# Performance work log

Measured on AMD Instinct MI355X. Metric: run time of the kernel, lower is better.

## Reference

```python
import jax, jax.numpy as jnp
import numpy as np

HIDDEN_DIM = 1024
NUM_HEADS = 16
HEAD_DIM = HIDDEN_DIM // NUM_HEADS
SCALAR_NORM = float(np.sqrt(HIDDEN_DIM / NUM_HEADS))


def setup_inputs() -> dict:
    key = jax.random.key(0)
    k1, k2 = jax.random.split(key)
    B, N, D = 2, 2048, HIDDEN_DIM
    x = jax.random.normal(k1, (B, N, D), dtype=jnp.float32)
    # torch Linear weight shape: (3D, D); xavier_uniform-like scale
    limit = float(np.sqrt(6.0 / (D + 3 * D)))
    W_qkv = jax.random.uniform(k2, (3 * D, D), dtype=jnp.float32, minval=-limit, maxval=limit)
    return {"x": x, "W_qkv": W_qkv}


def reference(x, W_qkv):
    b, n, d = x.shape
    h, hd = NUM_HEADS, HEAD_DIM
    qkv = x @ W_qkv.T  # (B, N, 3D)
    q, k, v = jnp.split(qkv, 3, axis=-1)
    # (B, H, N, hd)
    q = q.reshape(b, n, h, hd).transpose(0, 2, 1, 3)
    k = k.reshape(b, n, h, hd).transpose(0, 2, 1, 3)
    v = v.reshape(b, n, h, hd).transpose(0, 2, 1, 3)
    scores = jnp.einsum('bhik,bhjk->bhij', q, k) / SCALAR_NORM
    attn = jax.nn.softmax(scores, axis=-1)
    out = jnp.einsum('bhij,bhjk->bhik', attn, v)
    return out.transpose(0, 2, 1, 3).reshape(b, n, d)
```

## Files before the change

kernel.cpp:

```cpp
#include <hip/hip_runtime.h>
#include <hip/hip_bf16.h>

#define SEQ 2048
#define DMODEL 1024
#define NHEADS 16
#define HD 64
#define BATCH 2

typedef short bf16x8 __attribute__((ext_vector_type(8)));
typedef float f32x4 __attribute__((ext_vector_type(4)));
typedef float f32x16 __attribute__((ext_vector_type(16)));

static __device__ inline ushort f2bf(float f) {
    unsigned u = __float_as_uint(f);
    return (ushort)((u + 0x7fffu + ((u >> 16) & 1u)) >> 16);
}

static __device__ inline unsigned pk2bf(float a, float b) {
    __hip_bfloat162 h = __float22bfloat162_rn(make_float2(a, b));
    union { __hip_bfloat162 h; unsigned u; } c; c.h = h;
    return c.u;
}

static __device__ inline void async16(const ushort* g, ushort* l) {
    __builtin_amdgcn_global_load_lds((const __attribute__((address_space(1))) void*)g,
                                     (__attribute__((address_space(3))) void*)l, 16, 0, 0);
}

static __device__ inline void plane32swap(unsigned& a, unsigned& b) {
    asm volatile("v_permlane32_swap_b32 %0, %1" : "+v"(a), "+v"(b));
}

__global__ void cvt2(const float* __restrict__ a, ushort* __restrict__ da, int na,
                     const float* __restrict__ b, ushort* __restrict__ db, int nb) {
    long i = (long)(blockIdx.x * blockDim.x + threadIdx.x) * 4;
    const float* s; ushort* d;
    if (i < na) { s = a + i; d = da + i; }
    else { long j = i - na; if (j >= nb) return; s = b + j; d = db + j; }
    float4 v = *(const float4*)s;
    ushort4 o; o.x = f2bf(v.x); o.y = f2bf(v.y); o.z = f2bf(v.z); o.w = f2bf(v.w);
    *(ushort4*)d = o;
}

union GemmSmem {
    struct { ushort A[128 * 64]; ushort B[128 * 64]; } st;
    ushort C[128 * 128];
};

__global__ __launch_bounds__(256) void qkv_gemm(
        const ushort* __restrict__ X, const ushort* __restrict__ W,
        ushort* __restrict__ Qd, ushort* __restrict__ Kd, ushort* __restrict__ Vd) {
    __shared__ GemmSmem sm;
    const int t = threadIdx.x;
    const int lane = t & 63, l15 = lane & 15, quad = lane >> 4;
    const int w = t >> 6, wm = w >> 1, wn = w & 1;
    const int gm = blockIdx.x, gn = blockIdx.y;
    const int srow = t >> 3, scol = (t & 7) * 8;

    f32x4 acc[4][4] = {};

    for (int kt = 0; kt < 16; ++kt) {
        const int k0 = kt * 64;
        __syncthreads();
#pragma unroll
        for (int inst = 0; inst < 4; ++inst) {
            async16(&X[(gm * 128 + inst * 32 + srow) * 1024 + k0 + scol], &sm.st.A[inst * 2048 + t * 8]);
            async16(&W[(gn * 128 + inst * 32 + srow) * 1024 + k0 + scol], &sm.st.B[inst * 2048 + t * 8]);
        }
        __syncthreads();
#pragma unroll
        for (int ks = 0; ks < 2; ++ks) {
            const int kk = ks * 32 + quad * 8;
            bf16x8 af[4], bfr[4];
#pragma unroll
            for (int i = 0; i < 4; ++i) {
                af[i]  = *(const bf16x8*)&sm.st.A[(wm * 64 + i * 16 + l15) * 64 + kk];
                bfr[i] = *(const bf16x8*)&sm.st.B[(wn * 64 + i * 16 + l15) * 64 + kk];
            }
#pragma unroll
            for (int i = 0; i < 4; ++i)
#pragma unroll
                for (int j = 0; j < 4; ++j)
                    acc[i][j] = __builtin_amdgcn_mfma_f32_16x16x32_bf16(af[i], bfr[j], acc[i][j], 0, 0, 0);
        }
    }

    __syncthreads();
    const float sc = (gn < 8) ? (0.125f * 1.44269504f) : 1.0f;
#pragma unroll
    for (int i = 0; i < 4; ++i)
#pragma unroll
        for (int reg = 0; reg < 4; ++reg) {
            const int row = wm * 64 + i * 16 + quad * 4 + reg;
            const int sw = (row & 7) * 8;
#pragma unroll
            for (int jp = 0; jp < 4; jp += 2) {
                unsigned u = pk2bf(acc[i][jp][reg] * sc, acc[i][jp + 1][reg] * sc);
                sm.C[row * 128 + ((wn * 64 + jp * 16 + l15) ^ sw)] = (ushort)u;
                sm.C[row * 128 + ((wn * 64 + (jp + 1) * 16 + l15) ^ sw)] = (ushort)(u >> 16);
            }
        }
    __syncthreads();

    const int which = gn >> 3;
    ushort* dst = (which == 0) ? Qd : ((which == 1) ? Kd : Vd);
    const int rloc = t >> 4, l = t & 15;
#pragma unroll
    for (int pass = 0; pass < 8; ++pass) {
        const int r = pass * 16 + rloc;
        bf16x8 v = *(const bf16x8*)&sm.C[r * 128 + ((l * 8) ^ ((r & 7) * 8))];
        const int ng = gm * 128 + r;
        const int b = ng >> 11, n = ng & 2047;
        const int cl = (gn * 128 + l * 8) & 1023;
        const int h = cl >> 6, hd = cl & 63;
        *(bf16x8*)&dst[(((b * NHEADS + h) * SEQ) + n) * HD + hd] = v;
    }
}

__global__ __launch_bounds__(256) void tr_v(const ushort* __restrict__ src, ushort* __restrict__ dst) {
    __shared__ ushort sT[64][72];
    const int t = threadIdx.x;
    const int bh = blockIdx.y, nt = blockIdx.x;
    const int r0 = t >> 3, c8 = (t & 7) * 8;
    const ushort* sp = src + ((long)bh * SEQ + nt * 64) * HD;
#pragma unroll
    for (int rr = 0; rr < 64; rr += 32)
        *(bf16x8*)&sT[rr + r0][c8] = *(const bf16x8*)&sp[(rr + r0) * HD + c8];
    __syncthreads();
    ushort* dp = dst + (long)bh * HD * SEQ + nt * 64;
#pragma unroll
    for (int rr = 0; rr < 64; rr += 32) {
        const int hd = rr + r0;
        bf16x8 v;
#pragma unroll
        for (int j = 0; j < 8; ++j) v[j] = (short)sT[c8 + j][hd];
        *(bf16x8*)&dp[(long)hd * SEQ + c8] = v;
    }
}

__global__ __launch_bounds__(256, 1) void attn_kernel(
        const ushort* __restrict__ Q, const ushort* __restrict__ K,
        const ushort* __restrict__ VT, float* __restrict__ O) {
    __shared__ ushort sK[2][128 * 64];
    __shared__ ushort sVT[2][64 * 128];
    __shared__ float sL[4][64];

    const int t = threadIdx.x;
    const int lane = t & 63, l31 = lane & 31, hi = lane >> 5;
    const int w = t >> 6;

    const int flat = blockIdx.y * gridDim.x + blockIdx.x;
    const int qt = (flat >> 3) & 7;
    const int bh = (flat & 7) + ((flat >> 6) << 3);

    const ushort* Qp = Q + ((long)bh * SEQ + qt * 256 + w * 64) * HD;
    const ushort* Kp = K + (long)bh * SEQ * HD;
    const ushort* Vp = VT + (long)bh * HD * SEQ;

    bf16x8 bq[2][4];
#pragma unroll
    for (int qh = 0; qh < 2; ++qh)
#pragma unroll
        for (int ks = 0; ks < 4; ++ks)
            bq[qh][ks] = *(const bf16x8*)&Qp[(qh * 32 + l31) * HD + ks * 16 + hi * 8];

    const int krow = t >> 3;
    const int kcol = ((t & 7) ^ (krow & 7)) * 8;
    const ushort* gK = Kp + krow * HD + kcol;
    const int vrow = t >> 4;
    const int vcol = ((t & 15) ^ (vrow & 7)) * 8;
    const ushort* gV = Vp + (long)vrow * SEQ + vcol;

    ushort* lK[2] = { &sK[0][t * 8], &sK[1][t * 8] };
    ushort* lV[2] = { &sVT[0][t * 8], &sVT[1][t * 8] };

    f32x16 accA[2] = {}, accB[2] = {};
    f32x4 LpA = {}, LpB = {};
    const int swz = (l31 & 7) << 3;

#pragma unroll
    for (int c = 0; c < 4; ++c) {
        async16(gK + c * 32 * HD, lK[0] + c * 2048);
        async16(gV + (long)c * 16 * SEQ, lV[0] + c * 2048);
    }
    __syncthreads();

    for (int kt = 0; kt < 16; ++kt) {
        const int cur = kt & 1;
        if (kt < 15) {
            const ushort* nK = gK + (kt + 1) * 128 * HD;
            const ushort* nV = gV + (kt + 1) * 128;
#pragma unroll
            for (int c = 0; c < 4; ++c) {
                async16(nK + c * 32 * HD, lK[cur ^ 1] + c * 2048);
                async16(nV + (long)c * 16 * SEQ, lV[cur ^ 1] + c * 2048);
            }
        }
        const ushort* bK = sK[cur];
        const ushort* bV = sVT[cur];

        f32x16 sA[4], sB[4];
#pragma unroll
        for (int nb = 0; nb < 4; ++nb) {
            f32x16 zA = {}, zB = {};
#pragma unroll
            for (int ks = 0; ks < 4; ++ks) {
                bf16x8 ak = *(const bf16x8*)&bK[(nb * 32 + l31) * 64 + ((ks * 16 + hi * 8) ^ swz)];
                zA = __builtin_amdgcn_mfma_f32_32x32x16_bf16(ak, bq[0][ks], zA, 0, 0, 0);
                zB = __builtin_amdgcn_mfma_f32_32x32x16_bf16(ak, bq[1][ks], zB, 0, 0, 0);
            }
            sA[nb] = zA; sB[nb] = zB;
        }

#pragma unroll
        for (int h = 0; h < 2; ++h) {
            bf16x8 paA[4], paB[4];
#pragma unroll
            for (int nb2 = 0; nb2 < 2; ++nb2) {
                float pA[16], pB[16];
#pragma unroll
                for (int r = 0; r < 16; ++r) {
                    pA[r] = __builtin_amdgcn_exp2f(sA[h * 2 + nb2][r]);
                    pB[r] = __builtin_amdgcn_exp2f(sB[h * 2 + nb2][r]);
                }
#pragma unroll
                for (int r = 0; r < 16; ++r) { LpA[r & 3] += pA[r]; LpB[r & 3] += pB[r]; }
#pragma unroll
                for (int h2 = 0; h2 < 2; ++h2) {
                    const int b = 8 * h2;
                    unsigned a0 = pk2bf(pA[b + 0], pA[b + 1]);
                    unsigned a1 = pk2bf(pA[b + 2], pA[b + 3]);
                    unsigned a2 = pk2bf(pA[b + 4], pA[b + 5]);
                    unsigned a3 = pk2bf(pA[b + 6], pA[b + 7]);
                    plane32swap(a0, a2);
                    plane32swap(a1, a3);
                    union { unsigned u[4]; bf16x8 v; } fa;
                    fa.u[0] = a0; fa.u[1] = a1; fa.u[2] = a2; fa.u[3] = a3;
                    paA[nb2 * 2 + h2] = fa.v;
                    unsigned b0 = pk2bf(pB[b + 0], pB[b + 1]);
                    unsigned b1 = pk2bf(pB[b + 2], pB[b + 3]);
                    unsigned b2 = pk2bf(pB[b + 4], pB[b + 5]);
                    unsigned b3 = pk2bf(pB[b + 6], pB[b + 7]);
                    plane32swap(b0, b2);
                    plane32swap(b1, b3);
                    union { unsigned u[4]; bf16x8 v; } fb;
                    fb.u[0] = b0; fb.u[1] = b1; fb.u[2] = b2; fb.u[3] = b3;
                    paB[nb2 * 2 + h2] = fb.v;
                }
            }
#pragma unroll
            for (int db = 0; db < 2; ++db)
#pragma unroll
                for (int ks = 0; ks < 4; ++ks) {
                    bf16x8 vf = *(const bf16x8*)&bV[(db * 32 + l31) * 128 + h * 64 + ((ks * 16 + hi * 8) ^ swz)];
                    accA[db] = __builtin_amdgcn_mfma_f32_32x32x16_bf16(paA[ks], vf, accA[db], 0, 0, 0);
                    accB[db] = __builtin_amdgcn_mfma_f32_32x32x16_bf16(paB[ks], vf, accB[db], 0, 0, 0);
                }
        }

        __syncthreads();
    }

    {
        const float la = (LpA[0] + LpA[1]) + (LpA[2] + LpA[3]);
        unsigned lu = __float_as_uint(la), lv = lu;
        plane32swap(lu, lv);
        const float lb = (LpB[0] + LpB[1]) + (LpB[2] + LpB[3]);
        unsigned mu = __float_as_uint(lb), mv = mu;
        plane32swap(mu, mv);
        if (hi == 0) {
            sL[w][l31]      = __uint_as_float(lu) + __uint_as_float(lv);
            sL[w][32 + l31] = __uint_as_float(mu) + __uint_as_float(mv);
        }
    }
    __syncthreads();

    const int b = bh >> 4, h = bh & 15;
    const int qg0 = qt * 256 + w * 64;
#pragma unroll
    for (int r = 0; r < 16; ++r) {
        const int ql = (r & 3) + 8 * (r >> 2) + 4 * hi;
        const float invA = 1.0f / sL[w][ql];
        const float invB = 1.0f / sL[w][32 + ql];
#pragma unroll
        for (int db = 0; db < 2; ++db) {
            O[((long)b * SEQ + qg0 + ql) * DMODEL + h * HD + db * 32 + l31]      = accA[db][r] * invA;
            O[((long)b * SEQ + qg0 + 32 + ql) * DMODEL + h * HD + db * 32 + l31] = accB[db][r] * invB;
        }
    }
}

extern "C" void kernel_launch(void* const* d_in, const int* in_sizes, int n_in,
                              void* d_out, int out_size, void* d_ws, size_t ws_size,
                              hipStream_t stream) {
    const float* x  = (const float*)d_in[0];
    const float* Wq = (const float*)d_in[1];
    float* out = (float*)d_out;

    const int NX = BATCH * SEQ * DMODEL;
    const int NW = 3 * DMODEL * DMODEL;
    const int NQKV = BATCH * NHEADS * SEQ * HD;

    ushort* xb = (ushort*)d_ws;
    ushort* wb = xb + NX;
    ushort* q  = wb + NW;
    ushort* k  = q + NQKV;
    ushort* vtmp = k + NQKV;
    ushort* vt = xb;

    cvt2<<<(NX + NW) / 4 / 256, 256, 0, stream>>>(x, xb, NX, Wq, wb, NW);

    dim3 g1(4096 / 128, 3072 / 128);
    qkv_gemm<<<g1, 256, 0, stream>>>(xb, wb, q, k, vtmp);

    dim3 gt(SEQ / 64, BATCH * NHEADS);
    tr_v<<<gt, 256, 0, stream>>>(vtmp, vt);

    dim3 g2(SEQ / 256, BATCH * NHEADS);
    attn_kernel<<<g2, 256, 0, stream>>>(q, k, vt, out);
}
```

Before: 170.1 us.

## Triple-buffer K/V tiles and software-pipeline QK with softmax/PV

Moves K and V shared-memory staging from double to triple buffering, prefetching two tiles ahead with explicit vmcnt waits and raw s_barrier instead of __syncthreads. The loop is restructured so the QK^T MFMAs for the next tile are issued after the softmax and PV of the current tile, which lets the tensor work of one tile overlap the exp work of another. This is meant to hide global-load latency and the serialization between exp and MFMA phases within a single wave. In exchange it uses more LDS (48KB of K/V), holds all eight P fragments live, and raises register pressure. The final iterations redundantly refetch tile 15 to keep the vmcnt accounting uniform.

```diff
diff --git a/kernel.cpp b/kernel.cpp
--- a/kernel.cpp
+++ b/kernel.cpp
@@ -141,8 +141,8 @@
 __global__ __launch_bounds__(256, 1) void attn_kernel(
         const ushort* __restrict__ Q, const ushort* __restrict__ K,
         const ushort* __restrict__ VT, float* __restrict__ O) {
-    __shared__ ushort sK[2][128 * 64];
-    __shared__ ushort sVT[2][64 * 128];
+    __shared__ ushort sK[3][128 * 64];
+    __shared__ ushort sVT[3][64 * 128];
     __shared__ float sL[4][64];
 
     const int t = threadIdx.x;
@@ -171,35 +171,28 @@
     const int vcol = ((t & 15) ^ (vrow & 7)) * 8;
     const ushort* gV = Vp + (long)vrow * SEQ + vcol;
 
-    ushort* lK[2] = { &sK[0][t * 8], &sK[1][t * 8] };
-    ushort* lV[2] = { &sVT[0][t * 8], &sVT[1][t * 8] };
+    ushort* stK0 = &sK[0][t * 8]; ushort* stK1 = &sK[1][t * 8]; ushort* stK2 = &sK[2][t * 8];
+    ushort* stV0 = &sVT[0][t * 8]; ushort* stV1 = &sVT[1][t * 8]; ushort* stV2 = &sVT[2][t * 8];
+    const ushort* rdK0 = sK[0]; const ushort* rdK1 = sK[1]; const ushort* rdK2 = sK[2];
+    const ushort* rdV0 = sVT[0]; const ushort* rdV1 = sVT[1]; const ushort* rdV2 = sVT[2];
 
     f32x16 accA[2] = {}, accB[2] = {};
+    f32x16 sA[4], sB[4];
+    bf16x8 paA[8], paB[8];
     f32x4 LpA = {}, LpB = {};
     const int swz = (l31 & 7) << 3;
 
-#pragma unroll
-    for (int c = 0; c < 4; ++c) {
-        async16(gK + c * 32 * HD, lK[0] + c * 2048);
-        async16(gV + (long)c * 16 * SEQ, lV[0] + c * 2048);
-    }
-    __syncthreads();
-
-    for (int kt = 0; kt < 16; ++kt) {
-        const int cur = kt & 1;
-        if (kt < 15) {
-            const ushort* nK = gK + (kt + 1) * 128 * HD;
-            const ushort* nV = gV + (kt + 1) * 128;
-#pragma unroll
-            for (int c = 0; c < 4; ++c) {
-                async16(nK + c * 32 * HD, lK[cur ^ 1] + c * 2048);
-                async16(nV + (long)c * 16 * SEQ, lV[cur ^ 1] + c * 2048);
-            }
-        }
-        const ushort* bK = sK[cur];
-        const ushort* bV = sVT[cur];
-
-        f32x16 sA[4], sB[4];
+    auto do_stage = [&](int tile, ushort* dK, ushort* dV) {
+        const ushort* nK = gK + (long)tile * 128 * HD;
+        const ushort* nV = gV + tile * 128;
+#pragma unroll
+        for (int c = 0; c < 4; ++c) {
+            async16(nK + c * 32 * HD, dK + c * 2048);
+            async16(nV + (long)c * 16 * SEQ, dV + c * 2048);
+        }
+    };
+
+    auto do_qk = [&](const ushort* bK) {
 #pragma unroll
         for (int nb = 0; nb < 4; ++nb) {
             f32x16 zA = {}, zB = {};
@@ -211,55 +204,81 @@
             }
             sA[nb] = zA; sB[nb] = zB;
         }
-
-#pragma unroll
-        for (int h = 0; h < 2; ++h) {
-            bf16x8 paA[4], paB[4];
-#pragma unroll
-            for (int nb2 = 0; nb2 < 2; ++nb2) {
-                float pA[16], pB[16];
-#pragma unroll
-                for (int r = 0; r < 16; ++r) {
-                    pA[r] = __builtin_amdgcn_exp2f(sA[h * 2 + nb2][r]);
-                    pB[r] = __builtin_amdgcn_exp2f(sB[h * 2 + nb2][r]);
-                }
-#pragma unroll
-                for (int r = 0; r < 16; ++r) { LpA[r & 3] += pA[r]; LpB[r & 3] += pB[r]; }
-#pragma unroll
-                for (int h2 = 0; h2 < 2; ++h2) {
-                    const int b = 8 * h2;
-                    unsigned a0 = pk2bf(pA[b + 0], pA[b + 1]);
-                    unsigned a1 = pk2bf(pA[b + 2], pA[b + 3]);
-                    unsigned a2 = pk2bf(pA[b + 4], pA[b + 5]);
-                    unsigned a3 = pk2bf(pA[b + 6], pA[b + 7]);
-                    plane32swap(a0, a2);
-                    plane32swap(a1, a3);
-                    union { unsigned u[4]; bf16x8 v; } fa;
-                    fa.u[0] = a0; fa.u[1] = a1; fa.u[2] = a2; fa.u[3] = a3;
-                    paA[nb2 * 2 + h2] = fa.v;
-                    unsigned b0 = pk2bf(pB[b + 0], pB[b + 1]);
-                    unsigned b1 = pk2bf(pB[b + 2], pB[b + 3]);
-                    unsigned b2 = pk2bf(pB[b + 4], pB[b + 5]);
-                    unsigned b3 = pk2bf(pB[b + 6], pB[b + 7]);
-                    plane32swap(b0, b2);
-                    plane32swap(b1, b3);
-                    union { unsigned u[4]; bf16x8 v; } fb;
-                    fb.u[0] = b0; fb.u[1] = b1; fb.u[2] = b2; fb.u[3] = b3;
-                    paB[nb2 * 2 + h2] = fb.v;
-                }
-            }
+    };
+
+    auto do_sm = [&]() {
+#pragma unroll
+        for (int sb = 0; sb < 4; ++sb) {
+            float pA[16], pB[16];
+#pragma unroll
+            for (int r = 0; r < 16; ++r) {
+                pA[r] = __builtin_amdgcn_exp2f(sA[sb][r]);
+                pB[r] = __builtin_amdgcn_exp2f(sB[sb][r]);
+            }
+#pragma unroll
+            for (int r = 0; r < 16; ++r) { LpA[r & 3] += pA[r]; LpB[r & 3] += pB[r]; }
+#pragma unroll
+            for (int h2 = 0; h2 < 2; ++h2) {
+                const int b = 8 * h2;
+                const int flat = (sb >> 1) * 4 + (sb & 1) * 2 + h2;
+                unsigned a0 = pk2bf(pA[b + 0], pA[b + 1]);
+                unsigned a1 = pk2bf(pA[b + 2], pA[b + 3]);
+                unsigned a2 = pk2bf(pA[b + 4], pA[b + 5]);
+                unsigned a3 = pk2bf(pA[b + 6], pA[b + 7]);
+                plane32swap(a0, a2);
+                plane32swap(a1, a3);
+                union { unsigned u[4]; bf16x8 v; } fa;
+                fa.u[0] = a0; fa.u[1] = a1; fa.u[2] = a2; fa.u[3] = a3;
+                paA[flat] = fa.v;
+                unsigned b0 = pk2bf(pB[b + 0], pB[b + 1]);
+                unsigned b1 = pk2bf(pB[b + 2], pB[b + 3]);
+                unsigned b2 = pk2bf(pB[b + 4], pB[b + 5]);
+                unsigned b3 = pk2bf(pB[b + 6], pB[b + 7]);
+                plane32swap(b0, b2);
+                plane32swap(b1, b3);
+                union { unsigned u[4]; bf16x8 v; } fb;
+                fb.u[0] = b0; fb.u[1] = b1; fb.u[2] = b2; fb.u[3] = b3;
+                paB[flat] = fb.v;
+            }
+        }
+    };
+
+    auto do_pv = [&](const ushort* bV) {
+#pragma unroll
+        for (int h = 0; h < 2; ++h)
 #pragma unroll
             for (int db = 0; db < 2; ++db)
 #pragma unroll
                 for (int ks = 0; ks < 4; ++ks) {
                     bf16x8 vf = *(const bf16x8*)&bV[(db * 32 + l31) * 128 + h * 64 + ((ks * 16 + hi * 8) ^ swz)];
-                    accA[db] = __builtin_amdgcn_mfma_f32_32x32x16_bf16(paA[ks], vf, accA[db], 0, 0, 0);
-                    accB[db] = __builtin_amdgcn_mfma_f32_32x32x16_bf16(paB[ks], vf, accB[db], 0, 0, 0);
+                    accA[db] = __builtin_amdgcn_mfma_f32_32x32x16_bf16(paA[h * 4 + ks], vf, accA[db], 0, 0, 0);
+                    accB[db] = __builtin_amdgcn_mfma_f32_32x32x16_bf16(paB[h * 4 + ks], vf, accB[db], 0, 0, 0);
                 }
-        }
-
-        __syncthreads();
-    }
+    };
+
+    do_stage(0, stK0, stV0);
+    do_stage(1, stK1, stV1);
+    asm volatile("s_waitcnt vmcnt(8)" ::: "memory");
+    __builtin_amdgcn_s_barrier();
+    __builtin_amdgcn_sched_barrier(0);
+    do_qk(rdK0);
+
+    for (int kt = 0; kt < 15; ++kt) {
+        int ft = kt + 2; if (ft > 15) ft = 15;
+        do_stage(ft, stK2, stV2);
+        do_sm();
+        do_pv(rdV0);
+        asm volatile("s_waitcnt vmcnt(8)" ::: "memory");
+        __builtin_amdgcn_s_barrier();
+        __builtin_amdgcn_sched_barrier(0);
+        do_qk(rdK1);
+        ushort* tk = stK0; stK0 = stK1; stK1 = stK2; stK2 = tk;
+        ushort* tv = stV0; stV0 = stV1; stV1 = stV2; stV2 = tv;
+        const ushort* rk = rdK0; rdK0 = rdK1; rdK1 = rdK2; rdK2 = rk;
+        const ushort* rv = rdV0; rdV0 = rdV1; rdV1 = rdV2; rdV2 = rv;
+    }
+    do_sm();
+    do_pv(rdV0);
 
     {
         const float la = (LpA[0] + LpA[1]) + (LpA[2] + LpA[3]);
```

Result: faster. 165.8 us (-2.5%).

## Split attention KV range across two blocks and fuse V transpose into GEMM

Applied to the files above, without the earlier changes.

The QKV GEMM epilogue now writes V directly in transposed (head_dim x seq) layout, which removes the separate transpose kernel. Attention is split in two along the key dimension (split-K / flash-decoding style), doubling the grid to 512 blocks and allowing 2 blocks per CU. Each half writes unnormalized partial outputs and row sums, and a new combine kernel adds the halves and normalizes. This adds an extra fp32 output buffer and a full read/write pass over the output. The split is exact only because the softmax path uses no max subtraction, so the partial sums combine directly.

```diff
diff --git a/kernel.cpp b/kernel.cpp
--- a/kernel.cpp
+++ b/kernel.cpp
@@ -86,64 +86,69 @@
     }
 
     __syncthreads();
-    const float sc = (gn < 8) ? (0.125f * 1.44269504f) : 1.0f;
-#pragma unroll
-    for (int i = 0; i < 4; ++i)
-#pragma unroll
-        for (int reg = 0; reg < 4; ++reg) {
-            const int row = wm * 64 + i * 16 + quad * 4 + reg;
-            const int sw = (row & 7) * 8;
-#pragma unroll
-            for (int jp = 0; jp < 4; jp += 2) {
-                unsigned u = pk2bf(acc[i][jp][reg] * sc, acc[i][jp + 1][reg] * sc);
-                sm.C[row * 128 + ((wn * 64 + jp * 16 + l15) ^ sw)] = (ushort)u;
-                sm.C[row * 128 + ((wn * 64 + (jp + 1) * 16 + l15) ^ sw)] = (ushort)(u >> 16);
-            }
-        }
-    __syncthreads();
-
-    const int which = gn >> 3;
-    ushort* dst = (which == 0) ? Qd : ((which == 1) ? Kd : Vd);
-    const int rloc = t >> 4, l = t & 15;
-#pragma unroll
-    for (int pass = 0; pass < 8; ++pass) {
-        const int r = pass * 16 + rloc;
-        bf16x8 v = *(const bf16x8*)&sm.C[r * 128 + ((l * 8) ^ ((r & 7) * 8))];
-        const int ng = gm * 128 + r;
-        const int b = ng >> 11, n = ng & 2047;
-        const int cl = (gn * 128 + l * 8) & 1023;
-        const int h = cl >> 6, hd = cl & 63;
-        *(bf16x8*)&dst[(((b * NHEADS + h) * SEQ) + n) * HD + hd] = v;
-    }
-}
-
-__global__ __launch_bounds__(256) void tr_v(const ushort* __restrict__ src, ushort* __restrict__ dst) {
-    __shared__ ushort sT[64][72];
-    const int t = threadIdx.x;
-    const int bh = blockIdx.y, nt = blockIdx.x;
-    const int r0 = t >> 3, c8 = (t & 7) * 8;
-    const ushort* sp = src + ((long)bh * SEQ + nt * 64) * HD;
-#pragma unroll
-    for (int rr = 0; rr < 64; rr += 32)
-        *(bf16x8*)&sT[rr + r0][c8] = *(const bf16x8*)&sp[(rr + r0) * HD + c8];
-    __syncthreads();
-    ushort* dp = dst + (long)bh * HD * SEQ + nt * 64;
-#pragma unroll
-    for (int rr = 0; rr < 64; rr += 32) {
-        const int hd = rr + r0;
-        bf16x8 v;
-#pragma unroll
-        for (int j = 0; j < 8; ++j) v[j] = (short)sT[c8 + j][hd];
-        *(bf16x8*)&dp[(long)hd * SEQ + c8] = v;
-    }
-}
-
-__global__ __launch_bounds__(256, 1) void attn_kernel(
+    if (gn < 16) {
+        const float sc = (gn < 8) ? (0.125f * 1.44269504f) : 1.0f;
+#pragma unroll
+        for (int i = 0; i < 4; ++i)
+#pragma unroll
+            for (int reg = 0; reg < 4; ++reg) {
+                const int row = wm * 64 + i * 16 + quad * 4 + reg;
+                const int sw = (row & 7) * 8;
+#pragma unroll
+                for (int jp = 0; jp < 4; jp += 2) {
+                    unsigned u = pk2bf(acc[i][jp][reg] * sc, acc[i][jp + 1][reg] * sc);
+                    sm.C[row * 128 + ((wn * 64 + jp * 16 + l15) ^ sw)] = (ushort)u;
+                    sm.C[row * 128 + ((wn * 64 + (jp + 1) * 16 + l15) ^ sw)] = (ushort)(u >> 16);
+                }
+            }
+        __syncthreads();
+
+        ushort* dst = (gn < 8) ? Qd : Kd;
+        const int rloc = t >> 4, l = t & 15;
+#pragma unroll
+        for (int pass = 0; pass < 8; ++pass) {
+            const int r = pass * 16 + rloc;
+            bf16x8 v = *(const bf16x8*)&sm.C[r * 128 + ((l * 8) ^ ((r & 7) * 8))];
+            const int ng = gm * 128 + r;
+            const int b = ng >> 11, n = ng & 2047;
+            const int cl = (gn * 128 + l * 8) & 1023;
+            const int h = cl >> 6, hd = cl & 63;
+            *(bf16x8*)&dst[(((b * NHEADS + h) * SEQ) + n) * HD + hd] = v;
+        }
+    } else {
+#pragma unroll
+        for (int i = 0; i < 4; ++i)
+#pragma unroll
+            for (int reg = 0; reg < 4; ++reg) {
+                const int nloc = wm * 64 + i * 16 + quad * 4 + reg;
+#pragma unroll
+                for (int jp = 0; jp < 4; ++jp) {
+                    const int f = wn * 64 + jp * 16 + l15;
+                    sm.C[f * 128 + (nloc ^ ((f & 7) * 8))] = f2bf(acc[i][jp][reg]);
+                }
+            }
+        __syncthreads();
+
+        const int rloc = t >> 4, l = t & 15;
+        const int b = gm >> 4;
+        const int n0 = (gm & 15) * 128 + l * 8;
+#pragma unroll
+        for (int pass = 0; pass < 8; ++pass) {
+            const int r = pass * 16 + rloc;
+            bf16x8 v = *(const bf16x8*)&sm.C[r * 128 + ((l * 8) ^ ((r & 7) * 8))];
+            const int cl = (gn * 128 + r) & 1023;
+            const int h = cl >> 6, hd = cl & 63;
+            *(bf16x8*)&Vd[(((long)(b * NHEADS + h) * HD) + hd) * SEQ + n0] = v;
+        }
+    }
+}
+
+__global__ __launch_bounds__(256, 2) void attn_kernel(
         const ushort* __restrict__ Q, const ushort* __restrict__ K,
-        const ushort* __restrict__ VT, float* __restrict__ O) {
+        const ushort* __restrict__ VT, float* __restrict__ O0,
+        float* __restrict__ O1, float* __restrict__ Lbuf) {
     __shared__ ushort sK[2][128 * 64];
     __shared__ ushort sVT[2][64 * 128];
-    __shared__ float sL[4][64];
 
     const int t = threadIdx.x;
     const int lane = t & 63, l31 = lane & 31, hi = lane >> 5;
@@ -151,11 +156,12 @@
 
     const int flat = blockIdx.y * gridDim.x + blockIdx.x;
     const int qt = (flat >> 3) & 7;
-    const int bh = (flat & 7) + ((flat >> 6) << 3);
+    const int half = (flat >> 6) & 1;
+    const int bh = (flat & 7) + ((flat >> 7) << 3);
 
     const ushort* Qp = Q + ((long)bh * SEQ + qt * 256 + w * 64) * HD;
-    const ushort* Kp = K + (long)bh * SEQ * HD;
-    const ushort* Vp = VT + (long)bh * HD * SEQ;
+    const ushort* Kp = K + ((long)bh * SEQ + half * 1024) * HD;
+    const ushort* Vp = VT + (long)bh * HD * SEQ + half * 1024;
 
     bf16x8 bq[2][4];
 #pragma unroll
@@ -185,9 +191,9 @@
     }
     __syncthreads();
 
-    for (int kt = 0; kt < 16; ++kt) {
+    for (int kt = 0; kt < 8; ++kt) {
         const int cur = kt & 1;
-        if (kt < 15) {
+        if (kt < 7) {
             const ushort* nK = gK + (kt + 1) * 128 * HD;
             const ushort* nV = gV + (kt + 1) * 128;
 #pragma unroll
@@ -261,6 +267,8 @@
         __syncthreads();
     }
 
+    const int qg0 = qt * 256 + w * 64;
+    float* Lh = Lbuf + ((long)(half * 32 + bh) << 11);
     {
         const float la = (LpA[0] + LpA[1]) + (LpA[2] + LpA[3]);
         unsigned lu = __float_as_uint(la), lv = lu;
@@ -269,24 +277,42 @@
         unsigned mu = __float_as_uint(lb), mv = mu;
         plane32swap(mu, mv);
         if (hi == 0) {
-            sL[w][l31]      = __uint_as_float(lu) + __uint_as_float(lv);
-            sL[w][32 + l31] = __uint_as_float(mu) + __uint_as_float(mv);
-        }
-    }
-    __syncthreads();
-
+            Lh[qg0 + l31]      = __uint_as_float(lu) + __uint_as_float(lv);
+            Lh[qg0 + 32 + l31] = __uint_as_float(mu) + __uint_as_float(mv);
+        }
+    }
+
+    float* Od = half ? O1 : O0;
     const int b = bh >> 4, h = bh & 15;
-    const int qg0 = qt * 256 + w * 64;
 #pragma unroll
     for (int r = 0; r < 16; ++r) {
         const int ql = (r & 3) + 8 * (r >> 2) + 4 * hi;
-        const float invA = 1.0f / sL[w][ql];
-        const float invB = 1.0f / sL[w][32 + ql];
 #pragma unroll
         for (int db = 0; db < 2; ++db) {
-            O[((long)b * SEQ + qg0 + ql) * DMODEL + h * HD + db * 32 + l31]      = accA[db][r] * invA;
-            O[((long)b * SEQ + qg0 + 32 + ql) * DMODEL + h * HD + db * 32 + l31] = accB[db][r] * invB;
-        }
+            Od[((long)b * SEQ + qg0 + ql) * DMODEL + h * HD + db * 32 + l31]      = accA[db][r];
+            Od[((long)b * SEQ + qg0 + 32 + ql) * DMODEL + h * HD + db * 32 + l31] = accB[db][r];
+        }
+    }
+}
+
+__global__ __launch_bounds__(256) void combine(
+        float* __restrict__ O0, const float* __restrict__ O1,
+        const float* __restrict__ Lbuf) {
+    const int N4 = BATCH * SEQ * DMODEL / 4;
+    const int stride = gridDim.x * blockDim.x;
+    for (int i = blockIdx.x * blockDim.x + threadIdx.x; i < N4; i += stride) {
+        const int e = i * 4;
+        const int row = e >> 10;
+        const int b = row >> 11, n = row & 2047;
+        const int h = (e & 1023) >> 6;
+        const int bh = b * NHEADS + h;
+        const float l = Lbuf[((long)bh << 11) + n] + Lbuf[((long)(32 + bh) << 11) + n];
+        const float inv = 1.0f / l;
+        float4 a = *(const float4*)&O0[e];
+        const float4 c = *(const float4*)&O1[e];
+        a.x = (a.x + c.x) * inv; a.y = (a.y + c.y) * inv;
+        a.z = (a.z + c.z) * inv; a.w = (a.w + c.w) * inv;
+        *(float4*)&O0[e] = a;
     }
 }
 
@@ -305,17 +331,17 @@
     ushort* wb = xb + NX;
     ushort* q  = wb + NW;
     ushort* k  = q + NQKV;
-    ushort* vtmp = k + NQKV;
-    ushort* vt = xb;
+    ushort* vt = k + NQKV;
+    float*  o1 = (float*)(vt + NQKV);
+    float*  lb = o1 + NX;
 
     cvt2<<<(NX + NW) / 4 / 256, 256, 0, stream>>>(x, xb, NX, Wq, wb, NW);
 
     dim3 g1(4096 / 128, 3072 / 128);
-    qkv_gemm<<<g1, 256, 0, stream>>>(xb, wb, q, k, vtmp);
-
-    dim3 gt(SEQ / 64, BATCH * NHEADS);
-    tr_v<<<gt, 256, 0, stream>>>(vtmp, vt);
-
-    dim3 g2(SEQ / 256, BATCH * NHEADS);
-    attn_kernel<<<g2, 256, 0, stream>>>(q, k, vt, out);
-}
+    qkv_gemm<<<g1, 256, 0, stream>>>(xb, wb, q, k, vt);
+
+    dim3 g2(16, 32);
+    attn_kernel<<<g2, 256, 0, stream>>>(q, k, vt, out, o1, lb);
+
+    combine<<<1024, 256, 0, stream>>>(out, o1, lb);
+}
```

After: 191.8 us. 1.13x slower.
